# Optimization experiments

Hardware: AMD Instinct MI355X
Metric: run time of the kernel (lower is better)

Reference implementation:

```python
import jax, jax.numpy as jnp
import numpy as np


def setup_inputs() -> dict:
    key = jax.random.key(0)
    k1, k2 = jax.random.split(key)
    N, M, D = 8192, 8192, 3
    pred = jax.random.normal(k1, (N, D), dtype=jnp.float32)
    label = jax.random.normal(k2, (M, D), dtype=jnp.float32)
    return {"pred": pred, "label": label}


def reference(pred, label):
    # pairwise L2 distances: dis[n, m] = ||pred[n] - label[m]||_2
    diff = pred[:, None, :] - label[None, :, :]        # [N, M, D]
    dis = jnp.sqrt(jnp.sum(diff * diff, axis=2))       # [N, M]
    dis_xy = jnp.mean(jnp.min(dis, axis=1))            # for each x, nearest y
    dis_yx = jnp.mean(jnp.min(dis, axis=0))            # for each y, nearest x
    return dis_xy + dis_yx
```

## Files before the change

kernel.cpp:

```cpp
#include <hip/hip_runtime.h>
#include <math.h>

#define TPB 256
#define CH 16
#define CS 512

__global__ __launch_bounds__(TPB) void pairmin_kernel(
    const float* __restrict__ pred, const float* __restrict__ label,
    float* __restrict__ part, int N, int M) {
  const int dir = blockIdx.z;
  const float* __restrict__ q = dir ? label : pred;
  const float* __restrict__ r = dir ? pred : label;
  const int nq = dir ? M : N;
  const int nr = dir ? N : M;
  const int cs = nr / CH;

  __shared__ float4 sx[CS / 4], sy[CS / 4], sz[CS / 4];
  float* sxf = (float*)sx;
  float* syf = (float*)sy;
  float* szf = (float*)sz;

  const int t = threadIdx.x;

  const int rbase = blockIdx.y * cs;
  for (int k = t; k < cs * 3; k += TPB) {
    float v = r[rbase * 3 + k];
    int p = k / 3;
    int c = k - p * 3;
    if (c == 0) sxf[p] = v;
    else if (c == 1) syf[p] = v;
    else szf[p] = v;
  }
  __syncthreads();

  const int i = blockIdx.x * TPB + t;
  const float px = q[3 * i + 0];
  const float py = q[3 * i + 1];
  const float pz = q[3 * i + 2];

  float m0 = 3.4e38f, m1 = 3.4e38f, m2 = 3.4e38f, m3 = 3.4e38f;
#pragma unroll 2
  for (int j = 0; j < cs / 4; ++j) {
    float4 X = sx[j], Y = sy[j], Z = sz[j];
    float dx, dy, dz, d;
    dx = px - X.x; dy = py - Y.x; dz = pz - Z.x;
    d = dx * dx + dy * dy + dz * dz; m0 = fminf(m0, d);
    dx = px - X.y; dy = py - Y.y; dz = pz - Z.y;
    d = dx * dx + dy * dy + dz * dz; m1 = fminf(m1, d);
    dx = px - X.z; dy = py - Y.z; dz = pz - Z.z;
    d = dx * dx + dy * dy + dz * dz; m2 = fminf(m2, d);
    dx = px - X.w; dy = py - Y.w; dz = pz - Z.w;
    d = dx * dx + dy * dy + dz * dz; m3 = fminf(m3, d);
  }
  float m = fminf(fminf(m0, m1), fminf(m2, m3));

  const size_t off = dir ? (size_t)CH * (size_t)N : 0;
  part[off + (size_t)blockIdx.y * (size_t)nq + i] = m;
}

__global__ __launch_bounds__(TPB) void reduce_kernel(
    const float* __restrict__ part, float* __restrict__ bsums, int N, int M) {
  const int nbx = N / TPB;
  const int b = blockIdx.x;
  const int dir = (b >= nbx) ? 1 : 0;
  const int pb = dir ? (b - nbx) : b;
  const int nq = dir ? M : N;
  const size_t off = dir ? (size_t)CH * (size_t)N : 0;
  const int t = threadIdx.x;
  const int i = pb * TPB + t;

  float m = 3.4e38f;
#pragma unroll
  for (int c = 0; c < CH; ++c)
    m = fminf(m, part[off + (size_t)c * (size_t)nq + i]);
  float d = sqrtf(m);

  for (int o = 32; o >= 1; o >>= 1) d += __shfl_down(d, o);
  __shared__ float wsum[TPB / 64];
  if ((t & 63) == 0) wsum[t >> 6] = d;
  __syncthreads();
  if (t == 0) {
    float s = 0.f;
#pragma unroll
    for (int w = 0; w < TPB / 64; ++w) s += wsum[w];
    bsums[b] = s;
  }
}

__global__ void final_kernel(const float* __restrict__ bsums,
                             float* __restrict__ out,
                             int nbx, int nby, int N, int M) {
  const int t = threadIdx.x;
  float v0 = (t < nbx) ? bsums[t] : 0.0f;
  float v1 = (t < nby) ? bsums[nbx + t] : 0.0f;
  for (int o = 32; o >= 1; o >>= 1) {
    v0 += __shfl_down(v0, o);
    v1 += __shfl_down(v1, o);
  }
  if (t == 0) out[0] = v0 / (float)N + v1 / (float)M;
}

extern "C" void kernel_launch(void* const* d_in, const int* in_sizes, int n_in,
                              void* d_out, int out_size, void* d_ws, size_t ws_size,
                              hipStream_t stream) {
  const float* pred  = (const float*)d_in[0];
  const float* label = (const float*)d_in[1];
  const int N = in_sizes[0] / 3;
  const int M = in_sizes[1] / 3;

  float* part  = (float*)d_ws;
  float* bsums = part + (size_t)CH * (size_t)(N + M);

  const int nbx = N / TPB;
  const int nby = M / TPB;

  pairmin_kernel<<<dim3(nbx, CH, 2), TPB, 0, stream>>>(pred, label, part, N, M);
  reduce_kernel<<<nbx + nby, TPB, 0, stream>>>(part, bsums, N, M);
  final_kernel<<<1, 64, 0, stream>>>(bsums, (float*)d_out, nbx, nby, N, M);
}
```

Before: 84.32 us.

## Register-tile four queries per thread and vectorize AoS loads

Each thread now processes four query points against each group of four reference points, so every set of LDS values is reused across four queries. Reference and query points are loaded with float4 vector loads straight from the interleaved layout, dropping the SoA transpose. The chunk count rises to 64 to keep the block count unchanged. This enlarges the partial-min buffer and the reduce kernel's reads, and raises register use per thread.

```diff
diff --git a/kernel.cpp b/kernel.cpp
--- a/kernel.cpp
+++ b/kernel.cpp
@@ -2,8 +2,9 @@
 #include <math.h>
 
 #define TPB 256
-#define CH 16
-#define CS 512
+#define QPT 4
+#define CH  64
+#define CSR 128
 
 __global__ __launch_bounds__(TPB) void pairmin_kernel(
     const float* __restrict__ pred, const float* __restrict__ label,
@@ -15,47 +16,46 @@
   const int nr = dir ? N : M;
   const int cs = nr / CH;
 
-  __shared__ float4 sx[CS / 4], sy[CS / 4], sz[CS / 4];
-  float* sxf = (float*)sx;
-  float* syf = (float*)sy;
-  float* szf = (float*)sz;
-
+  __shared__ float s[CSR * 3];
   const int t = threadIdx.x;
-
-  const int rbase = blockIdx.y * cs;
-  for (int k = t; k < cs * 3; k += TPB) {
-    float v = r[rbase * 3 + k];
-    int p = k / 3;
-    int c = k - p * 3;
-    if (c == 0) sxf[p] = v;
-    else if (c == 1) syf[p] = v;
-    else szf[p] = v;
-  }
+  if (t < (cs * 3) / 4)
+    ((float4*)s)[t] = ((const float4*)(r + (size_t)blockIdx.y * cs * 3))[t];
   __syncthreads();
 
-  const int i = blockIdx.x * TPB + t;
-  const float px = q[3 * i + 0];
-  const float py = q[3 * i + 1];
-  const float pz = q[3 * i + 2];
+  const int i0 = (blockIdx.x * TPB + t) * QPT;
+  const float4 Q0 = *(const float4*)(q + (size_t)i0 * 3 + 0);
+  const float4 Q1 = *(const float4*)(q + (size_t)i0 * 3 + 4);
+  const float4 Q2 = *(const float4*)(q + (size_t)i0 * 3 + 8);
+  const float px[QPT] = {Q0.x, Q0.w, Q1.z, Q2.y};
+  const float py[QPT] = {Q0.y, Q1.x, Q1.w, Q2.z};
+  const float pz[QPT] = {Q0.z, Q1.y, Q2.x, Q2.w};
 
-  float m0 = 3.4e38f, m1 = 3.4e38f, m2 = 3.4e38f, m3 = 3.4e38f;
+  float m[QPT] = {3.4e38f, 3.4e38f, 3.4e38f, 3.4e38f};
+
 #pragma unroll 2
   for (int j = 0; j < cs / 4; ++j) {
-    float4 X = sx[j], Y = sy[j], Z = sz[j];
-    float dx, dy, dz, d;
-    dx = px - X.x; dy = py - Y.x; dz = pz - Z.x;
-    d = dx * dx + dy * dy + dz * dz; m0 = fminf(m0, d);
-    dx = px - X.y; dy = py - Y.y; dz = pz - Z.y;
-    d = dx * dx + dy * dy + dz * dz; m1 = fminf(m1, d);
-    dx = px - X.z; dy = py - Y.z; dz = pz - Z.z;
-    d = dx * dx + dy * dy + dz * dz; m2 = fminf(m2, d);
-    dx = px - X.w; dy = py - Y.w; dz = pz - Z.w;
-    d = dx * dx + dy * dy + dz * dz; m3 = fminf(m3, d);
+    const float4 A = ((const float4*)s)[3 * j + 0];
+    const float4 B = ((const float4*)s)[3 * j + 1];
+    const float4 C = ((const float4*)s)[3 * j + 2];
+    const float rx[4] = {A.x, A.w, B.z, C.y};
+    const float ry[4] = {A.y, B.x, B.w, C.z};
+    const float rz[4] = {A.z, B.y, C.x, C.w};
+#pragma unroll
+    for (int rr = 0; rr < 4; ++rr) {
+#pragma unroll
+      for (int qq = 0; qq < QPT; ++qq) {
+        const float dx = px[qq] - rx[rr];
+        const float dy = py[qq] - ry[rr];
+        const float dz = pz[qq] - rz[rr];
+        const float d = dx * dx + dy * dy + dz * dz;
+        m[qq] = fminf(m[qq], d);
+      }
+    }
   }
-  float m = fminf(fminf(m0, m1), fminf(m2, m3));
 
   const size_t off = dir ? (size_t)CH * (size_t)N : 0;
-  part[off + (size_t)blockIdx.y * (size_t)nq + i] = m;
+  *(float4*)&part[off + (size_t)blockIdx.y * nq + i0] =
+      make_float4(m[0], m[1], m[2], m[3]);
 }
 
 __global__ __launch_bounds__(TPB) void reduce_kernel(
@@ -72,7 +72,7 @@
   float m = 3.4e38f;
 #pragma unroll
   for (int c = 0; c < CH; ++c)
-    m = fminf(m, part[off + (size_t)c * (size_t)nq + i]);
+    m = fminf(m, part[off + (size_t)c * nq + i]);
   float d = sqrtf(m);
 
   for (int o = 32; o >= 1; o >>= 1) d += __shfl_down(d, o);
@@ -80,10 +80,10 @@
   if ((t & 63) == 0) wsum[t >> 6] = d;
   __syncthreads();
   if (t == 0) {
-    float s = 0.f;
+    float sum = 0.f;
 #pragma unroll
-    for (int w = 0; w < TPB / 64; ++w) s += wsum[w];
-    bsums[b] = s;
+    for (int w = 0; w < TPB / 64; ++w) sum += wsum[w];
+    bsums[b] = sum;
   }
 }
 
@@ -114,7 +114,8 @@
   const int nbx = N / TPB;
   const int nby = M / TPB;
 
-  pairmin_kernel<<<dim3(nbx, CH, 2), TPB, 0, stream>>>(pred, label, part, N, M);
+  pairmin_kernel<<<dim3(N / (TPB * QPT), CH, 2), TPB, 0, stream>>>(
+      pred, label, part, N, M);
   reduce_kernel<<<nbx + nby, TPB, 0, stream>>>(part, bsums, N, M);
   final_kernel<<<1, 64, 0, stream>>>(bsums, (float*)d_out, nbx, nby, N, M);
 }
```

Measured after the change: 81.81 us. -3.0%, faster.
